# Performance work log

Measured on AMD Instinct MI355X. Metric: run time of the kernel, lower is better.

Reference implementation:

```python
import jax, jax.numpy as jnp
import numpy as np
from numpy.polynomial import Polynomial

B, C = 2000000, 10
EXP = dict(start=0.0, stop=1.0, n=1000, deg=8)
INV = dict(start=10.0, stop=30.0, n=1000, deg=4)
LOG = dict(start=0.01, stop=0.5, n=1000, deg=8)
ITERATIONS = 3


def _fit(fn, start, stop, n, deg):
    x = np.linspace(start, stop, n)
    return Polynomial.fit(x, fn(x), deg).convert(kind=Polynomial).coef.astype(np.float32)


def _polyval(coeffs, x):
    # Horner; coeffs ascending order (numpy Polynomial convention)
    res = jnp.full_like(x, coeffs[-1])
    for i in range(coeffs.shape[0] - 2, -1, -1):
        res = res * x + coeffs[i]
    return res


def setup_inputs() -> dict:
    key = jax.random.key(0)
    k1, k2 = jax.random.split(key)
    enc_input = jax.random.uniform(k1, (B, C), dtype=jnp.float32)  # logits in [0,1)
    labels = jax.random.randint(k2, (B,), 0, C)
    enc_target = jax.nn.one_hot(labels, C, dtype=jnp.float32)
    exp_coeffs = jnp.asarray(_fit(np.exp, **{'start': EXP['start'], 'stop': EXP['stop'], 'n': EXP['n'], 'deg': EXP['deg']}))
    inverse_coeffs = jnp.asarray(_fit(lambda x: 1.0 / x, INV['start'], INV['stop'], INV['n'], INV['deg']))
    log_coeffs = jnp.asarray(_fit(np.log, LOG['start'], LOG['stop'], LOG['n'], LOG['deg']))
    return {
        'enc_input': enc_input,
        'enc_target': enc_target,
        'exp_coeffs': exp_coeffs,
        'inverse_coeffs': inverse_coeffs,
        'log_coeffs': log_coeffs,
        'iterations': ITERATIONS,
    }


def reference(enc_input, enc_target, exp_coeffs, inverse_coeffs, log_coeffs, iterations):
    # exp via polynomial approximation (Horner / ciphertext poly eval)
    e = _polyval(exp_coeffs, enc_input)                      # [B, C]
    s = jnp.sum(e, axis=1, keepdims=True)                    # [B, 1]
    # inverse via polynomial initial guess + Newton-Raphson refinement
    inv = _polyval(inverse_coeffs, s)
    for _ in range(iterations):
        inv = inv * (2.0 - s * inv)
    softmax = e * inv                                        # [B, C]
    log_softmax = _polyval(log_coeffs, softmax)              # [B, C]
    # mean cross-entropy over the batch
    loss = -jnp.sum(enc_target * log_softmax) / enc_input.shape[0]
    return loss


if __name__ == '__main__':
    out = reference(**setup_inputs())
    print(out)
```

## Files before the change

### kernel.cpp

```cpp
#include <hip/hip_runtime.h>

#define CCOL 10
#define TPB 256
#define NBLOCKS 1024

typedef float v4f __attribute__((ext_vector_type(4)));
#define NT(p) __builtin_nontemporal_load(p)

__device__ __forceinline__ float horner9(const float c[9], float x) {
    float v = c[8];
#pragma unroll
    for (int i = 7; i >= 0; i--) v = fmaf(v, x, c[i]);
    return v;
}

#define EXP4(v, base)                          \
    e[(base) + 0] = horner9(ec, (v).x);        \
    e[(base) + 1] = horner9(ec, (v).y);        \
    e[(base) + 2] = horner9(ec, (v).z);        \
    e[(base) + 3] = horner9(ec, (v).w);

#define LOG4(tv, base)                                                    \
    {                                                                     \
        float i0 = ((base) + 0 < CCOL) ? inv0 : inv1;                     \
        float i1 = ((base) + 1 < CCOL) ? inv0 : inv1;                     \
        float i2 = ((base) + 2 < CCOL) ? inv0 : inv1;                     \
        float i3 = ((base) + 3 < CCOL) ? inv0 : inv1;                     \
        local = fmaf((tv).x, horner9(lc, e[(base) + 0] * i0), local);     \
        local = fmaf((tv).y, horner9(lc, e[(base) + 1] * i1), local);     \
        local = fmaf((tv).z, horner9(lc, e[(base) + 2] * i2), local);     \
        local = fmaf((tv).w, horner9(lc, e[(base) + 3] * i3), local);     \
    }

__global__ __launch_bounds__(TPB, 4) void ce_kernel(
    const float* __restrict__ x, const float* __restrict__ tgt,
    const float* __restrict__ exp_c, const float* __restrict__ inv_c,
    const float* __restrict__ log_c, const int* __restrict__ iters_p,
    float* __restrict__ partials, int npairs, int nchunks)
{
    __shared__ v4f lds4[2560];

    float ec[9], ic[5], lc[9];
#pragma unroll
    for (int i = 0; i < 9; i++) ec[i] = exp_c[i];
#pragma unroll
    for (int i = 0; i < 5; i++) ic[i] = inv_c[i];
#pragma unroll
    for (int i = 0; i < 9; i++) lc[i] = log_c[i];
    const int niter = iters_p[0];

    const int tid  = threadIdx.x;
    const int lane = tid & 63;
    const int w    = tid >> 6;
    const int wg   = blockIdx.x * 4 + w;
    const int W    = gridDim.x * 4;

    v4f* lx = lds4 + w * 640;
    v4f* lt = lx + 320;
    const v4f* bx = (const v4f*)((const float*)lx + lane * 20);
    const v4f* bt = (const v4f*)((const float*)lt + lane * 20);

    float local = 0.0f;

    int q = wg;
    v4f rx0, rx1, rx2, rx3, rx4, rt0, rt1, rt2, rt3, rt4;
    if (q < nchunks) {
        const v4f* gx = (const v4f*)x   + (size_t)q * 320 + lane;
        const v4f* gt = (const v4f*)tgt + (size_t)q * 320 + lane;
        rx0 = NT(gx); rx1 = NT(gx + 64); rx2 = NT(gx + 128); rx3 = NT(gx + 192); rx4 = NT(gx + 256);
        rt0 = NT(gt); rt1 = NT(gt + 64); rt2 = NT(gt + 128); rt3 = NT(gt + 192); rt4 = NT(gt + 256);
    }

    while (q < nchunks) {
        v4f* sx = lx + lane;
        sx[0] = rx0; sx[64] = rx1; sx[128] = rx2; sx[192] = rx3; sx[256] = rx4;
        v4f* st = lt + lane;
        st[0] = rt0; st[64] = rt1; st[128] = rt2; st[192] = rt3; st[256] = rt4;

        int qn = q + W;
        if (qn < nchunks) {
            const v4f* gx = (const v4f*)x   + (size_t)qn * 320 + lane;
            const v4f* gt = (const v4f*)tgt + (size_t)qn * 320 + lane;
            rx0 = NT(gx); rx1 = NT(gx + 64); rx2 = NT(gx + 128); rx3 = NT(gx + 192); rx4 = NT(gx + 256);
            rt0 = NT(gt); rt1 = NT(gt + 64); rt2 = NT(gt + 128); rt3 = NT(gt + 192); rt4 = NT(gt + 256);
        }

        v4f a0 = bx[0], a1 = bx[1], a2 = bx[2], a3 = bx[3], a4 = bx[4];
        float e[2 * CCOL];
        EXP4(a0, 0) EXP4(a1, 4) EXP4(a2, 8) EXP4(a3, 12) EXP4(a4, 16)

        float s0 = 0.0f, s1 = 0.0f;
#pragma unroll
        for (int i = 0; i < CCOL; i++) s0 += e[i];
#pragma unroll
        for (int i = CCOL; i < 2 * CCOL; i++) s1 += e[i];

        float inv0 = ic[4], inv1 = ic[4];
#pragma unroll
        for (int k = 3; k >= 0; k--) {
            inv0 = fmaf(inv0, s0, ic[k]);
            inv1 = fmaf(inv1, s1, ic[k]);
        }
        for (int k = 0; k < niter; k++) {
            inv0 = inv0 * (2.0f - s0 * inv0);
            inv1 = inv1 * (2.0f - s1 * inv1);
        }

        v4f t0 = bt[0], t1 = bt[1], t2 = bt[2], t3 = bt[3], t4 = bt[4];
        LOG4(t0, 0) LOG4(t1, 4) LOG4(t2, 8) LOG4(t3, 12) LOG4(t4, 16)

        q = qn;
    }

    int tail0 = nchunks * 64;
    for (int p = tail0 + blockIdx.x * TPB + tid; p < npairs; p += gridDim.x * TPB) {
        const float* xp = x   + (size_t)p * 2 * CCOL;
        const float* tp = tgt + (size_t)p * 2 * CCOL;
#pragma unroll
        for (int r = 0; r < 2; r++) {
            float e2[CCOL], s = 0.0f;
#pragma unroll
            for (int c = 0; c < CCOL; c++) {
                float v = horner9(ec, xp[r * CCOL + c]);
                e2[c] = v; s += v;
            }
            float inv = ic[4];
#pragma unroll
            for (int k = 3; k >= 0; k--) inv = fmaf(inv, s, ic[k]);
            for (int k = 0; k < niter; k++) inv = inv * (2.0f - s * inv);
#pragma unroll
            for (int c = 0; c < CCOL; c++)
                local = fmaf(tp[r * CCOL + c], horner9(lc, e2[c] * inv), local);
        }
    }

#pragma unroll
    for (int off = 32; off > 0; off >>= 1)
        local += __shfl_down(local, off, 64);

    __syncthreads();
    float* wsum = (float*)lds4;
    if (lane == 0) wsum[w] = local;
    __syncthreads();
    if (tid == 0)
        partials[blockIdx.x] = wsum[0] + wsum[1] + wsum[2] + wsum[3];
}

__global__ __launch_bounds__(TPB) void reduce_kernel(
    const float* __restrict__ partials, float* __restrict__ out, float neg_inv_b)
{
    int tid = threadIdx.x;
    float local = 0.0f;
#pragma unroll
    for (int k = 0; k < NBLOCKS / TPB; k++)
        local += partials[tid + k * TPB];
#pragma unroll
    for (int off = 32; off > 0; off >>= 1)
        local += __shfl_down(local, off, 64);
    __shared__ float wsum[4];
    if ((tid & 63) == 0) wsum[tid >> 6] = local;
    __syncthreads();
    if (tid == 0)
        out[0] = (wsum[0] + wsum[1] + wsum[2] + wsum[3]) * neg_inv_b;
}

extern "C" void kernel_launch(void* const* d_in, const int* in_sizes, int n_in,
                              void* d_out, int out_size, void* d_ws, size_t ws_size,
                              hipStream_t stream) {
    const float* x  = (const float*)d_in[0];
    const float* t  = (const float*)d_in[1];
    const float* ec = (const float*)d_in[2];
    const float* ic = (const float*)d_in[3];
    const float* lc = (const float*)d_in[4];
    const int*   it = (const int*)d_in[5];
    float* out = (float*)d_out;
    float* partials = (float*)d_ws;

    int b_rows = in_sizes[0] / CCOL;
    int npairs = b_rows / 2;
    int nchunks = npairs / 64;
    float neg_inv_b = -1.0f / (float)b_rows;

    ce_kernel<<<NBLOCKS, TPB, 0, stream>>>(x, t, ec, ic, lc, it, partials,
                                           npairs, nchunks);
    reduce_kernel<<<1, TPB, 0, stream>>>(partials, out, neg_inv_b);
}
```

Measured before the change: 169.1 us.

## Compute exp on coalesced registers and share only pair sums and inverses through LDS

Each lane now evaluates the exp polynomial directly on the coalesced vectors it loaded, instead of first staging the raw inputs and targets through LDS and re-reading them row-aligned. Only partial pair sums are written to LDS so each lane can assemble two row sums and their inverses. The inverses go back to LDS, and each lane gathers the per-element inverse it needs through precomputed row pointers. Target prefetch is also delayed until after the exp phase to lower live register pressure. The aim is to cut LDS traffic and bandwidth, at the cost of extra indexed gathers and reliance on wavefront-synchronous LDS ordering without barriers.

```diff
diff --git a/kernel.cpp b/kernel.cpp
--- a/kernel.cpp
+++ b/kernel.cpp
@@ -5,7 +5,9 @@
 #define NBLOCKS 1024
 
 typedef float v4f __attribute__((ext_vector_type(4)));
+typedef float v2f __attribute__((ext_vector_type(2)));
 #define NT(p) __builtin_nontemporal_load(p)
+
 
 __device__ __forceinline__ float horner9(const float c[9], float x) {
     float v = c[8];
@@ -20,17 +22,11 @@
     e[(base) + 2] = horner9(ec, (v).z);        \
     e[(base) + 3] = horner9(ec, (v).w);
 
-#define LOG4(tv, base)                                                    \
-    {                                                                     \
-        float i0 = ((base) + 0 < CCOL) ? inv0 : inv1;                     \
-        float i1 = ((base) + 1 < CCOL) ? inv0 : inv1;                     \
-        float i2 = ((base) + 2 < CCOL) ? inv0 : inv1;                     \
-        float i3 = ((base) + 3 < CCOL) ? inv0 : inv1;                     \
-        local = fmaf((tv).x, horner9(lc, e[(base) + 0] * i0), local);     \
-        local = fmaf((tv).y, horner9(lc, e[(base) + 1] * i1), local);     \
-        local = fmaf((tv).z, horner9(lc, e[(base) + 2] * i2), local);     \
-        local = fmaf((tv).w, horner9(lc, e[(base) + 3] * i3), local);     \
-    }
+#define LOGDOT(tv, base, i0v, i1v)                                        \
+    local = fmaf((tv).x, horner9(lc, e[(base) + 0] * (i0v)), local);      \
+    local = fmaf((tv).y, horner9(lc, e[(base) + 1] * (i0v)), local);      \
+    local = fmaf((tv).z, horner9(lc, e[(base) + 2] * (i1v)), local);      \
+    local = fmaf((tv).w, horner9(lc, e[(base) + 3] * (i1v)), local);
 
 __global__ __launch_bounds__(TPB, 4) void ce_kernel(
     const float* __restrict__ x, const float* __restrict__ tgt,
@@ -38,7 +34,7 @@
     const float* __restrict__ log_c, const int* __restrict__ iters_p,
     float* __restrict__ partials, int npairs, int nchunks)
 {
-    __shared__ v4f lds4[2560];
+    __shared__ __align__(16) float lds[4 * 1024];
 
     float ec[9], ic[5], lc[9];
 #pragma unroll
@@ -55,10 +51,31 @@
     const int wg   = blockIdx.x * 4 + w;
     const int W    = gridDim.x * 4;
 
-    v4f* lx = lds4 + w * 640;
-    v4f* lt = lx + 320;
-    const v4f* bx = (const v4f*)((const float*)lx + lane * 20);
-    const v4f* bt = (const v4f*)((const float*)lt + lane * 20);
+    float* const part = lds + w * 1024;
+    float* const linv = part + 640;
+
+    const float* pa0; const float* pa1; const float* pb0; const float* pb1;
+    const float* pc0; const float* pc1; const float* pd0; const float* pd1;
+    const float* pe0; const float* pe1;
+    {
+        int r0[5], r1[5];
+#pragma unroll
+        for (int k = 0; k < 5; k++) {
+            int b = 256 * k + 4 * lane;
+            int r = b / 10;
+            int pos = b - 10 * r;
+            r0[k] = r;
+            r1[k] = r + (pos == 8 ? 1 : 0);
+        }
+        pa0 = linv + r0[0]; pa1 = linv + r1[0];
+        pb0 = linv + r0[1]; pb1 = linv + r1[1];
+        pc0 = linv + r0[2]; pc1 = linv + r1[2];
+        pd0 = linv + r0[3]; pd1 = linv + r1[3];
+        pe0 = linv + r0[4]; pe1 = linv + r1[4];
+    }
+    v2f* const pw  = (v2f*)(part + 2 * lane);
+    v2f* const rs  = (v2f*)(part + 10 * lane);
+    v2f* const ivw = (v2f*)(linv + 2 * lane);
 
     float local = 0.0f;
 
@@ -72,43 +89,54 @@
     }
 
     while (q < nchunks) {
-        v4f* sx = lx + lane;
-        sx[0] = rx0; sx[64] = rx1; sx[128] = rx2; sx[192] = rx3; sx[256] = rx4;
-        v4f* st = lt + lane;
-        st[0] = rt0; st[64] = rt1; st[128] = rt2; st[192] = rt3; st[256] = rt4;
-
         int qn = q + W;
-        if (qn < nchunks) {
-            const v4f* gx = (const v4f*)x   + (size_t)qn * 320 + lane;
-            const v4f* gt = (const v4f*)tgt + (size_t)qn * 320 + lane;
-            rx0 = NT(gx); rx1 = NT(gx + 64); rx2 = NT(gx + 128); rx3 = NT(gx + 192); rx4 = NT(gx + 256);
-            rt0 = NT(gt); rt1 = NT(gt + 64); rt2 = NT(gt + 128); rt3 = NT(gt + 192); rt4 = NT(gt + 256);
-        }
-
-        v4f a0 = bx[0], a1 = bx[1], a2 = bx[2], a3 = bx[3], a4 = bx[4];
+        bool pf = (qn < nchunks);
+        v4f nx0, nx1, nx2, nx3, nx4, nt0, nt1, nt2, nt3, nt4;
+        const v4f* gx = (const v4f*)x   + (size_t)qn * 320 + lane;
+        const v4f* gt = (const v4f*)tgt + (size_t)qn * 320 + lane;
+        if (pf) {
+            nx0 = NT(gx); nx1 = NT(gx + 64); nx2 = NT(gx + 128); nx3 = NT(gx + 192); nx4 = NT(gx + 256);
+        }
+
         float e[2 * CCOL];
-        EXP4(a0, 0) EXP4(a1, 4) EXP4(a2, 8) EXP4(a3, 12) EXP4(a4, 16)
-
-        float s0 = 0.0f, s1 = 0.0f;
-#pragma unroll
-        for (int i = 0; i < CCOL; i++) s0 += e[i];
-#pragma unroll
-        for (int i = CCOL; i < 2 * CCOL; i++) s1 += e[i];
-
-        float inv0 = ic[4], inv1 = ic[4];
-#pragma unroll
-        for (int k = 3; k >= 0; k--) {
-            inv0 = fmaf(inv0, s0, ic[k]);
-            inv1 = fmaf(inv1, s1, ic[k]);
-        }
+        EXP4(rx0, 0) EXP4(rx1, 4) EXP4(rx2, 8) EXP4(rx3, 12) EXP4(rx4, 16)
+        pw[0]   = (v2f){e[0]  + e[1],  e[2]  + e[3]};
+        pw[64]  = (v2f){e[4]  + e[5],  e[6]  + e[7]};
+        pw[128] = (v2f){e[8]  + e[9],  e[10] + e[11]};
+        pw[192] = (v2f){e[12] + e[13], e[14] + e[15]};
+        pw[256] = (v2f){e[16] + e[17], e[18] + e[19]};
+
+        v2f p0 = rs[0], p1 = rs[1], p2 = rs[2], p3 = rs[3], p4 = rs[4];
+        float sA = p0.x + p0.y + p1.x + p1.y + p2.x;
+        float sB = p2.y + p3.x + p3.y + p4.x + p4.y;
+        float iA = ic[4], iB = ic[4];
+#pragma unroll
+        for (int k = 3; k >= 0; k--) { iA = fmaf(iA, sA, ic[k]); iB = fmaf(iB, sB, ic[k]); }
         for (int k = 0; k < niter; k++) {
-            inv0 = inv0 * (2.0f - s0 * inv0);
-            inv1 = inv1 * (2.0f - s1 * inv1);
-        }
-
-        v4f t0 = bt[0], t1 = bt[1], t2 = bt[2], t3 = bt[3], t4 = bt[4];
-        LOG4(t0, 0) LOG4(t1, 4) LOG4(t2, 8) LOG4(t3, 12) LOG4(t4, 16)
-
+            iA = iA * (2.0f - sA * iA);
+            iB = iB * (2.0f - sB * iB);
+        }
+        ivw[0] = (v2f){iA, iB};
+
+        if (pf) {
+            nt0 = NT(gt); nt1 = NT(gt + 64); nt2 = NT(gt + 128); nt3 = NT(gt + 192); nt4 = NT(gt + 256);
+        }
+
+        float i00 = *pa0, i10 = *pa1;
+        float i01 = *pb0, i11 = *pb1;
+        float i02 = *pc0, i12 = *pc1;
+        float i03 = *pd0, i13 = *pd1;
+        float i04 = *pe0, i14 = *pe1;
+
+        LOGDOT(rt0, 0,  i00, i10)
+        LOGDOT(rt1, 4,  i01, i11)
+        LOGDOT(rt2, 8,  i02, i12)
+        LOGDOT(rt3, 12, i03, i13)
+        LOGDOT(rt4, 16, i04, i14)
+
+        if (!pf) break;
+        rx0 = nx0; rx1 = nx1; rx2 = nx2; rx3 = nx3; rx4 = nx4;
+        rt0 = nt0; rt1 = nt1; rt2 = nt2; rt3 = nt3; rt4 = nt4;
         q = qn;
     }
 
@@ -139,7 +167,7 @@
         local += __shfl_down(local, off, 64);
 
     __syncthreads();
-    float* wsum = (float*)lds4;
+    float* wsum = lds;
     if (lane == 0) wsum[w] = local;
     __syncthreads();
     if (tid == 0)
```

New measurement: 171.3 us. No clear change (+1.3%).
